# Kernel tuning notes

Measured on AMD Instinct MI355X. Metric: run time of the kernel, lower is better.

Reference implementation:

```python
import jax, jax.numpy as jnp
import numpy as np

N_HEAD, D_MODEL, DQ, DK, DV = 16, 1024, 64, 64, 64
B, LQ, LK = 2, 2048, 2048
EPS = 1e-3


def setup_inputs() -> dict:
    key = jax.random.key(0)
    ks = jax.random.split(key, 8)
    v = jax.random.normal(ks[0], (B, LK, D_MODEL), jnp.float32)
    k = jax.random.normal(ks[1], (B, LK, D_MODEL), jnp.float32)
    q = jax.random.normal(ks[2], (B, LQ, D_MODEL), jnp.float32)
    mask = jax.random.randint(ks[3], (B, LQ, LK), 0, 2).astype(bool)
    # xavier_normal for [n_head, d_model, d*]: fan_in=d_model, fan_out=d* (per torch, last two dims)
    def xav(kk, shape):
        std = np.sqrt(2.0 / (shape[-2] + shape[-1]))
        return jax.random.normal(kk, shape, jnp.float32) * std
    w_q = xav(ks[4], (N_HEAD, D_MODEL, DQ))
    w_k = xav(ks[5], (N_HEAD, D_MODEL, DK))
    w_v = xav(ks[6], (N_HEAD, D_MODEL, DV))
    # output linear: torch default init; use uniform(-1/sqrt(fan_in), ..)
    fan_in = N_HEAD * DV
    bound = 1.0 / np.sqrt(fan_in)
    kw, kb = jax.random.split(ks[7])
    w_o = jax.random.uniform(kw, (fan_in, D_MODEL), jnp.float32, -bound, bound)
    b_o = jax.random.uniform(kb, (D_MODEL,), jnp.float32, -bound, bound)
    gamma = jnp.ones((D_MODEL,), jnp.float32)
    beta = jnp.zeros((D_MODEL,), jnp.float32)
    return {"v": v, "k": k, "q": q, "mask": mask, "w_q": w_q, "w_k": w_k,
            "w_v": w_v, "w_o": w_o, "b_o": b_o, "gamma": gamma, "beta": beta}


def _layer_norm(x, gamma, beta):
    mean = jnp.mean(x, axis=-1, keepdims=True)
    # torch.std default is unbiased (ddof=1); eps added to std (not var)
    std = jnp.std(x, axis=-1, keepdims=True, ddof=1)
    return (x - mean) / (std + EPS) * gamma + beta


def reference(v, k, q, mask, w_q, w_k, w_v, w_o, b_o, gamma, beta):
    residual = k  # source uses k as residual
    # per-head projections: [h, b, l, d*]
    qh = jnp.einsum('bld,hde->hble', q, w_q)
    kh = jnp.einsum('bld,hde->hble', k, w_k)
    vh = jnp.einsum('bld,hde->hble', v, w_v)
    scale = 1.0 / np.sqrt(DK)
    scores = jnp.einsum('hbqe,hbke->hbqk', qh, kh) * scale  # [h,b,Lq,Lk]
    scores = jnp.where(mask[None], -jnp.inf, scores)
    attn = jax.nn.softmax(scores, axis=-1)
    out = jnp.einsum('hbqk,hbke->hbqe', attn, vh)  # [h,b,Lq,dv]
    # cat(split(out, batch, dim=0), dim=-1): heads concatenated on last dim
    out = out.transpose(1, 2, 0, 3).reshape(out.shape[1], out.shape[2], -1)
    out = out @ w_o + b_o
    x = out + residual  # dropout is identity in eval
    return _layer_norm(x, gamma, beta)
```

## Files before the change

### kernel.cpp

```cpp
#include <hip/hip_runtime.h>
#include <math.h>

typedef __bf16 bf16_t;
typedef bf16_t bf16x8 __attribute__((ext_vector_type(8)));
typedef float  f32x4  __attribute__((ext_vector_type(4)));
typedef unsigned short u16;
typedef u16 ushortx4 __attribute__((ext_vector_type(4)));
typedef unsigned long long u64;

#define MFMA16(a, b, c) __builtin_amdgcn_mfma_f32_16x16x32_bf16((a), (b), (c), 0, 0, 0)

__device__ __forceinline__ u16 f2bf(float f) {
    unsigned int u = __float_as_uint(f);
    u = (u + 0x7fffu + ((u >> 16) & 1u)) >> 16;
    return (u16)u;
}

__device__ __forceinline__ void gld16(const u16* g, u16* l) {
    __builtin_amdgcn_global_load_lds(
        (const __attribute__((address_space(1))) void*)g,
        (__attribute__((address_space(3))) void*)l, 16, 0, 0);
}


__global__ __launch_bounds__(256) void k_cvt3(const float* __restrict__ q,
                                              const float* __restrict__ k,
                                              const float* __restrict__ v,
                                              u16* __restrict__ qb,
                                              u16* __restrict__ kb,
                                              u16* __restrict__ vb) {
    int i = blockIdx.x * 256 + threadIdx.x;
    int sel = blockIdx.y;
    const float* src = sel == 0 ? q : (sel == 1 ? k : v);
    u16* dst = sel == 0 ? qb : (sel == 1 ? kb : vb);
    float4 val = ((const float4*)src)[i];
    ushortx4 r;
    r[0] = f2bf(val.x); r[1] = f2bf(val.y); r[2] = f2bf(val.z); r[3] = f2bf(val.w);
    ((ushortx4*)dst)[i] = r;
}

__global__ __launch_bounds__(256) void k_tcvt3(const float* __restrict__ w_q,
                                               const float* __restrict__ w_k,
                                               const float* __restrict__ w_v,
                                               u16* __restrict__ wqt,
                                               u16* __restrict__ wkt,
                                               u16* __restrict__ wvt) {
    __shared__ float tile[32][33];
    int z = blockIdx.z, h = z & 15, sel = z >> 4;
    const float* src = (sel == 0 ? w_q : (sel == 1 ? w_k : w_v));
    u16* dst = (sel == 0 ? wqt : (sel == 1 ? wkt : wvt));
    int r0 = blockIdx.x * 32, c0 = blockIdx.y * 32;
    int tx = threadIdx.x & 31, ty = threadIdx.x >> 5;
    const float* s = src + ((size_t)h * 1024 + r0) * 64 + c0;
#pragma unroll
    for (int i = 0; i < 4; ++i) tile[ty + i * 8][tx] = s[(ty + i * 8) * 64 + tx];
    __syncthreads();
    u16* d = dst + ((size_t)h * 64 + c0) * 1024 + r0;
#pragma unroll
    for (int i = 0; i < 4; ++i) d[(ty + i * 8) * 1024 + tx] = f2bf(tile[tx][ty + i * 8]);
}

__global__ __launch_bounds__(256) void k_tcvt(const float* __restrict__ src,
                                              u16* __restrict__ dst, int R, int C) {
    __shared__ float tile[32][33];
    int r0 = blockIdx.x * 32, c0 = blockIdx.y * 32;
    int tx = threadIdx.x & 31, ty = threadIdx.x >> 5;
    const float* s = src + (size_t)r0 * C + c0;
#pragma unroll
    for (int i = 0; i < 4; ++i) tile[ty + i * 8][tx] = s[(ty + i * 8) * (size_t)C + tx];
    __syncthreads();
    u16* d = dst + (size_t)c0 * R + r0;
#pragma unroll
    for (int i = 0; i < 4; ++i) d[(ty + i * 8) * (size_t)R + tx] = f2bf(tile[tx][ty + i * 8]);
}

__global__ __launch_bounds__(256) void k_packmask(const int* __restrict__ mask,
                                                  u64* __restrict__ mask64) {
    int bid = blockIdx.x;
    int ktg = bid & 7, q4 = (bid >> 3) & 511, b = bid >> 12;
    int wave = threadIdx.x >> 6, lane = threadIdx.x & 63;
    int q = q4 * 4 + wave;
    const int* mp = mask + ((size_t)(b * 2048 + q)) * 2048 + ktg * 256 + lane;
#pragma unroll
    for (int i = 0; i < 4; ++i) {
        int m = mp[i * 64];
        u64 bal = __ballot(m != 0);
        if (lane == 0) mask64[((size_t)(b * 32 + ktg * 4 + i)) * 2048 + q] = bal;
    }
}

#define GEMM_CORE(Ablk, Bblk, ACC)                                                    \
    int c0 = wave * 2;                                                                \
    const u16* Ag0 = Ablk + (size_t)(c0 * 16 + l15) * 1024 + quad * 8;                \
    const u16* Ag1 = Ablk + (size_t)((c0 + 1) * 16 + l15) * 1024 + quad * 8;          \
    const u16* Bg0 = Bblk + (size_t)(c0 * 16 + l15) * 1024 + quad * 8;                \
    const u16* Bg1 = Bblk + (size_t)((c0 + 1) * 16 + l15) * 1024 + quad * 8;          \
    gld16(Ag0, As + c0 * 512); gld16(Ag1, As + (c0 + 1) * 512);                       \
    gld16(Bg0, Bs + c0 * 512); gld16(Bg1, Bs + (c0 + 1) * 512);                       \
    __syncthreads();                                                                  \
    int buf = 0;                                                                      \
    for (int ks = 0; ks < 32; ++ks) {                                                 \
        if (ks < 31) {                                                                \
            int k0 = (ks + 1) * 32;                                                   \
            gld16(Ag0 + k0, As + (buf ^ 1) * 4096 + c0 * 512);                        \
            gld16(Ag1 + k0, As + (buf ^ 1) * 4096 + (c0 + 1) * 512);                  \
            gld16(Bg0 + k0, Bs + (buf ^ 1) * 4096 + c0 * 512);                        \
            gld16(Bg1 + k0, Bs + (buf ^ 1) * 4096 + (c0 + 1) * 512);                  \
        }                                                                             \
        bf16x8 af[4], bfr[4];                                                         \
        _Pragma("unroll")                                                             \
        for (int i = 0; i < 4; ++i)                                                   \
            af[i] = *(const bf16x8*)(As + buf * 4096 + (wy * 4 + i) * 512 + lane * 8);\
        _Pragma("unroll")                                                             \
        for (int j = 0; j < 4; ++j)                                                   \
            bfr[j] = *(const bf16x8*)(Bs + buf * 4096 + (wx * 4 + j) * 512 + lane * 8);\
        _Pragma("unroll")                                                             \
        for (int i = 0; i < 4; ++i)                                                   \
            _Pragma("unroll")                                                         \
            for (int j = 0; j < 4; ++j) ACC[i][j] = MFMA16(af[i], bfr[j], ACC[i][j]); \
        __syncthreads();                                                              \
        buf ^= 1;                                                                     \
    }

__global__ __launch_bounds__(256) void k_proj(
    const u16* __restrict__ qb, const u16* __restrict__ kb, const u16* __restrict__ vb,
    const u16* __restrict__ wqt, const u16* __restrict__ wkt, const u16* __restrict__ wvt,
    u16* __restrict__ oq, u16* __restrict__ okh, u16* __restrict__ ovt) {
    __shared__ __align__(16) u16 smem[18432];
    u16* As = smem;
    u16* Bs = smem + 8192;
    int z = blockIdx.y, gx = blockIdx.x;
    int bm, bn;
    const u16 *A, *B;
    if (z == 0)      { bm = gx >> 3; bn = gx & 7; A = qb; B = wqt; }
    else if (z == 1) { bm = gx >> 3; bn = gx & 7; A = kb; B = wkt; }
    else             { bm = gx & 7; bn = gx >> 3; A = wvt; B = vb; }
    A += (size_t)bm * 128 * 1024;
    B += (size_t)bn * 128 * 1024;
    int tid = threadIdx.x, wave = tid >> 6, lane = tid & 63;
    int wy = wave >> 1, wx = wave & 1, l15 = lane & 15, quad = lane >> 4;
    f32x4 acc[4][4] = {};
    GEMM_CORE(A, B, acc)
    u16* ep = smem + wave * 4608;
    float mulf = (z == 0) ? 0.18033688011112042f : 1.0f;
#pragma unroll
    for (int i = 0; i < 4; ++i)
#pragma unroll
        for (int j = 0; j < 4; ++j)
#pragma unroll
            for (int r = 0; r < 4; ++r)
                ep[(i * 16 + quad * 4 + r) * 72 + j * 16 + l15] = f2bf(acc[i][j][r] * mulf);
    int rl = lane >> 3, cg = lane & 7;
    if (z < 2) {
        int hh = bn * 2 + wx;
        int m0 = bm * 128 + wy * 64;
        int bb = m0 >> 11, l0 = m0 & 2047;
        u16* O = (z ? okh : oq) + ((size_t)((hh * 2 + bb) * 2048 + l0)) * 64;
#pragma unroll
        for (int s = 0; s < 8; ++s) {
            int row = s * 8 + rl;
            uint4 v = *(const uint4*)(ep + row * 72 + cg * 8);
            *(uint4*)(O + (size_t)row * 64 + cg * 8) = v;
        }
    } else {
        int m0 = bm * 128 + wy * 64;
        int hh = m0 >> 6;
        int n0 = bn * 128 + wx * 64;
        int bb = n0 >> 11, l0 = n0 & 2047;
        u16* O = ovt + (size_t)(hh * 2 + bb) * 131072 + (size_t)(m0 & 63) * 2048 + l0;
#pragma unroll
        for (int s = 0; s < 8; ++s) {
            int row = s * 8 + rl;
            uint4 v = *(const uint4*)(ep + row * 72 + cg * 8);
            *(uint4*)(O + (size_t)row * 2048 + cg * 8) = v;
        }
    }
}

__global__ __launch_bounds__(256) void k_out(
    const u16* __restrict__ ao, const u16* __restrict__ wot,
    const float* __restrict__ bo, const float* __restrict__ resid,
    float* __restrict__ xb) {
    __shared__ __align__(16) u16 smem[18432];
    u16* As = smem;
    u16* Bs = smem + 8192;
    int gx = blockIdx.x, bm = gx >> 3, bn = gx & 7;
    const u16* A = ao + (size_t)bm * 128 * 1024;
    const u16* B = wot + (size_t)bn * 128 * 1024;
    int tid = threadIdx.x, wave = tid >> 6, lane = tid & 63;
    int wy = wave >> 1, wx = wave & 1, l15 = lane & 15, quad = lane >> 4;
    f32x4 acc[4][4] = {};
    GEMM_CORE(A, B, acc)
    float* epf = (float*)(smem) + wave * 2176;
    int cgf = lane & 15, rlf = lane >> 4;
    int mbase = bm * 128 + wy * 64, nbase = bn * 128 + wx * 64;
#pragma unroll
    for (int cc = 0; cc < 2; ++cc) {
#pragma unroll
        for (int i2 = 0; i2 < 2; ++i2)
#pragma unroll
            for (int j = 0; j < 4; ++j)
#pragma unroll
                for (int r = 0; r < 4; ++r)
                    epf[(i2 * 16 + quad * 4 + r) * 68 + j * 16 + l15] =
                        acc[cc * 2 + i2][j][r];
#pragma unroll
        for (int s = 0; s < 8; ++s) {
            int row = s * 4 + rlf;
            f32x4 v = *(const f32x4*)(epf + row * 68 + cgf * 4);
            int m = mbase + cc * 32 + row, n = nbase + cgf * 4;
            float4 rsd = *(const float4*)(resid + (size_t)m * 1024 + n);
            float4 bo4 = *(const float4*)(bo + n);
            float4 o;
            o.x = v[0] + bo4.x + rsd.x;
            o.y = v[1] + bo4.y + rsd.y;
            o.z = v[2] + bo4.z + rsd.z;
            o.w = v[3] + bo4.w + rsd.w;
            *(float4*)(xb + (size_t)m * 1024 + n) = o;
        }
    }
}

__global__ __launch_bounds__(512) void k_attn(
    const u16* __restrict__ qh, const u16* __restrict__ kh,
    const u16* __restrict__ vt, const u64* __restrict__ mask64,
    u16* __restrict__ ao) {
    int qt = blockIdx.x, hb = blockIdx.y;
    int h = hb >> 1, b = hb & 1;
    int tid = threadIdx.x, wave = tid >> 6, lane = tid & 63;
    int l15 = lane & 15, quad = lane >> 4;

    __shared__ __align__(16) u16 Ks[2][4096], Vs[2][4096];
    __shared__ __align__(16) u16 Pb[8][16][72];

    int qrow0 = qt * 128 + wave * 16;
    const u16* Qp = qh + ((size_t)(hb * 2048) + qrow0 + l15) * 64 + quad * 8;
    bf16x8 qf0 = *(const bf16x8*)Qp;
    bf16x8 qf1 = *(const bf16x8*)(Qp + 32);

    int tK = wave >> 1, hK = wave & 1;
    const u16* Kg = kh + (size_t)hb * 131072 + (size_t)(tK * 16 + l15) * 64 + hK * 32 + quad * 8;
    const u16* Vg = vt + (size_t)hb * 131072 + (size_t)(tK * 16 + l15) * 2048 + hK * 32 + quad * 8;
    const u64* Mp = mask64 + (size_t)b * 65536 + qrow0 + l15;

    float l_lane = 0.f;
    f32x4 o[4] = {};

    gld16(Kg, &Ks[0][wave * 512]);
    gld16(Vg, &Vs[0][wave * 512]);
    u64 mw_cur = Mp[0];
    __syncthreads();
    int buf = 0;
    for (int kt = 0; kt < 32; ++kt) {
        u64 mw_nxt = 0;
        if (kt < 31) {
            gld16(Kg + (size_t)(kt + 1) * 4096, &Ks[buf ^ 1][wave * 512]);
            gld16(Vg + (size_t)(kt + 1) * 64, &Vs[buf ^ 1][wave * 512]);
            mw_nxt = Mp[(size_t)(kt + 1) * 2048];
        }
        f32x4 st[4] = {};
#pragma unroll
        for (int t = 0; t < 4; ++t) {
            bf16x8 k0 = *(const bf16x8*)&Ks[buf][(t * 2 + 0) * 512 + lane * 8];
            bf16x8 k1 = *(const bf16x8*)&Ks[buf][(t * 2 + 1) * 512 + lane * 8];
            st[t] = MFMA16(k0, qf0, st[t]);
            st[t] = MFMA16(k1, qf1, st[t]);
        }
        unsigned int w0 = (unsigned int)(mw_cur >> (quad * 4));
        unsigned int w1 = (unsigned int)(mw_cur >> (32 + quad * 4));
#pragma unroll
        for (int r = 0; r < 4; ++r) {
            st[0][r] = ((w0 >> r) & 1u) ? -3e30f : st[0][r];
            st[1][r] = ((w0 >> (16 + r)) & 1u) ? -3e30f : st[1][r];
            st[2][r] = ((w1 >> r) & 1u) ? -3e30f : st[2][r];
            st[3][r] = ((w1 >> (16 + r)) & 1u) ? -3e30f : st[3][r];
        }
#pragma unroll
        for (int t = 0; t < 4; ++t) {
            float p0 = __builtin_amdgcn_exp2f(st[t][0]);
            float p1 = __builtin_amdgcn_exp2f(st[t][1]);
            float p2 = __builtin_amdgcn_exp2f(st[t][2]);
            float p3 = __builtin_amdgcn_exp2f(st[t][3]);
            l_lane += (p0 + p1) + (p2 + p3);
            uint2 pk;
            pk.x = (__float_as_uint(p1) & 0xffff0000u) | (__float_as_uint(p0) >> 16);
            pk.y = (__float_as_uint(p3) & 0xffff0000u) | (__float_as_uint(p2) >> 16);
            *(uint2*)&Pb[wave][l15][t * 16 + quad * 4] = pk;
        }
#pragma unroll
        for (int kc = 0; kc < 2; ++kc) {
            bf16x8 pf = *(const bf16x8*)&Pb[wave][l15][kc * 32 + quad * 8];
#pragma unroll
            for (int t = 0; t < 4; ++t) {
                bf16x8 vf = *(const bf16x8*)&Vs[buf][(t * 2 + kc) * 512 + lane * 8];
                o[t] = MFMA16(pf, vf, o[t]);
            }
        }
        mw_cur = mw_nxt;
        __syncthreads();
        buf ^= 1;
    }
    float ls = l_lane;
    ls += __shfl_xor(ls, 16, 64);
    ls += __shfl_xor(ls, 32, 64);
    float inv = 1.0f / ls;
    f32x4 ivr;
#pragma unroll
    for (int r = 0; r < 4; ++r) ivr[r] = __shfl(inv, quad * 4 + r, 16);
#pragma unroll
    for (int t = 0; t < 4; ++t)
#pragma unroll
        for (int r = 0; r < 4; ++r)
            Pb[wave][quad * 4 + r][t * 16 + l15] = f2bf(o[t][r] * ivr[r]);
    int rl = lane >> 3, cg = lane & 7;
#pragma unroll
    for (int s = 0; s < 2; ++s) {
        int row = s * 8 + rl;
        uint4 v = *(const uint4*)&Pb[wave][row][cg * 8];
        *(uint4*)(ao + ((size_t)(b * 2048 + qrow0 + row)) * 1024 + h * 64 + cg * 8) = v;
    }
}

__global__ __launch_bounds__(256) void k_ln(const float* __restrict__ x,
                                            const float* __restrict__ gamma,
                                            const float* __restrict__ beta,
                                            float* __restrict__ out) {
    int row = blockIdx.x;
    const float* xr = x + (size_t)row * 1024;
    float4 v = ((const float4*)xr)[threadIdx.x];
    float s = v.x + v.y + v.z + v.w;
    float ss = v.x * v.x + v.y * v.y + v.z * v.z + v.w * v.w;
#pragma unroll
    for (int off = 32; off; off >>= 1) {
        s += __shfl_down(s, off, 64);
        ss += __shfl_down(ss, off, 64);
    }
    __shared__ float sb[8];
    int wave = threadIdx.x >> 6, lane = threadIdx.x & 63;
    if (lane == 0) { sb[wave] = s; sb[4 + wave] = ss; }
    __syncthreads();
    s = sb[0] + sb[1] + sb[2] + sb[3];
    ss = sb[4] + sb[5] + sb[6] + sb[7];
    float mean = s * (1.0f / 1024.0f);
    float var = fmaxf((ss - 1024.0f * mean * mean) * (1.0f / 1023.0f), 0.f);
    float inv = 1.0f / (sqrtf(var) + 1e-3f);
    float4 g = ((const float4*)gamma)[threadIdx.x];
    float4 bt = ((const float4*)beta)[threadIdx.x];
    float4 o;
    o.x = (v.x - mean) * inv * g.x + bt.x;
    o.y = (v.y - mean) * inv * g.y + bt.y;
    o.z = (v.z - mean) * inv * g.z + bt.z;
    o.w = (v.w - mean) * inv * g.w + bt.w;
    ((float4*)(out + (size_t)row * 1024))[threadIdx.x] = o;
}

extern "C" void kernel_launch(void* const* d_in, const int* in_sizes, int n_in,
                              void* d_out, int out_size, void* d_ws, size_t ws_size,
                              hipStream_t stream) {
    const float* v_in  = (const float*)d_in[0];
    const float* k_in  = (const float*)d_in[1];
    const float* q_in  = (const float*)d_in[2];
    const int*   mask  = (const int*)d_in[3];
    const float* w_q   = (const float*)d_in[4];
    const float* w_k   = (const float*)d_in[5];
    const float* w_v   = (const float*)d_in[6];
    const float* w_o   = (const float*)d_in[7];
    const float* b_o   = (const float*)d_in[8];
    const float* gamma = (const float*)d_in[9];
    const float* beta  = (const float*)d_in[10];
    float* out = (float*)d_out;

    char* ws = (char*)d_ws;
    const size_t MB = 1ull << 20;
    u16* qb  = (u16*)(ws + 0 * MB);
    u16* kb  = (u16*)(ws + 8 * MB);
    u16* vb  = (u16*)(ws + 16 * MB);
    u16* wqt = (u16*)(ws + 24 * MB);
    u16* wkt = (u16*)(ws + 26 * MB);
    u16* wvt = (u16*)(ws + 28 * MB);
    u16* wot = (u16*)(ws + 30 * MB);
    u16* qh  = (u16*)(ws + 32 * MB);
    u16* kh  = (u16*)(ws + 40 * MB);
    u16* vt  = (u16*)(ws + 48 * MB);
    u16* ao  = (u16*)(ws + 56 * MB);
    u64* mask64 = (u64*)(ws + 64 * MB);
    float* xb = (float*)(ws + 64 * MB);

    k_cvt3<<<dim3(4096, 3), dim3(256), 0, stream>>>(q_in, k_in, v_in, qb, kb, vb);
    k_tcvt3<<<dim3(32, 2, 48), dim3(256), 0, stream>>>(w_q, w_k, w_v, wqt, wkt, wvt);
    k_tcvt<<<dim3(32, 32), dim3(256), 0, stream>>>(w_o, wot, 1024, 1024);
    k_packmask<<<dim3(8192), dim3(256), 0, stream>>>(mask, mask64);
    k_proj<<<dim3(256, 3), dim3(256), 0, stream>>>(qb, kb, vb, wqt, wkt, wvt, qh, kh, vt);
    k_attn<<<dim3(16, 32), dim3(512), 0, stream>>>(qh, kh, vt, mask64, ao);
    k_out<<<dim3(256), dim3(256), 0, stream>>>(ao, wot, b_o, k_in, xb);
    k_ln<<<dim3(4096), dim3(256), 0, stream>>>(xb, gamma, beta, out);
}
```

Measured before the change: 303.2 us.

## Process two query row-tiles per wave in attention to reuse K/V fragments

The attention kernel now runs 4 waves per block instead of 8, and each wave handles 32 query rows as two 16-row halves. K and V fragments are loaded from LDS into registers once per key tile and reused for both halves, which roughly halves LDS read traffic per query row. Each wave issues twice as many global-to-LDS loads. The cost is higher register pressure and fewer waves per block to hide latency, which could lower occupancy.

```diff
diff --git a/kernel.cpp b/kernel.cpp
--- a/kernel.cpp
+++ b/kernel.cpp
@@ -221,7 +221,7 @@
     }
 }
 
-__global__ __launch_bounds__(512) void k_attn(
+__global__ __launch_bounds__(256) void k_attn(
     const u16* __restrict__ qh, const u16* __restrict__ kh,
     const u16* __restrict__ vt, const u64* __restrict__ mask64,
     u16* __restrict__ ao) {
@@ -231,94 +231,119 @@
     int l15 = lane & 15, quad = lane >> 4;
 
     __shared__ __align__(16) u16 Ks[2][4096], Vs[2][4096];
-    __shared__ __align__(16) u16 Pb[8][16][72];
-
-    int qrow0 = qt * 128 + wave * 16;
+    __shared__ __align__(16) u16 Pb[4][2][16][72];
+
+    int qrow0 = qt * 128 + wave * 32;
     const u16* Qp = qh + ((size_t)(hb * 2048) + qrow0 + l15) * 64 + quad * 8;
-    bf16x8 qf0 = *(const bf16x8*)Qp;
-    bf16x8 qf1 = *(const bf16x8*)(Qp + 32);
-
-    int tK = wave >> 1, hK = wave & 1;
-    const u16* Kg = kh + (size_t)hb * 131072 + (size_t)(tK * 16 + l15) * 64 + hK * 32 + quad * 8;
-    const u16* Vg = vt + (size_t)hb * 131072 + (size_t)(tK * 16 + l15) * 2048 + hK * 32 + quad * 8;
+    bf16x8 qf[2][2];
+    qf[0][0] = *(const bf16x8*)Qp;
+    qf[0][1] = *(const bf16x8*)(Qp + 32);
+    qf[1][0] = *(const bf16x8*)(Qp + 1024);
+    qf[1][1] = *(const bf16x8*)(Qp + 1024 + 32);
+
+    int c0 = wave * 2;
+    int rA = (c0 >> 1) * 16 + l15, dA = (c0 & 1) * 32 + quad * 8;
+    int rB = ((c0 + 1) >> 1) * 16 + l15, dB = ((c0 + 1) & 1) * 32 + quad * 8;
+    const u16* Kg0 = kh + (size_t)hb * 131072 + (size_t)rA * 64 + dA;
+    const u16* Kg1 = kh + (size_t)hb * 131072 + (size_t)rB * 64 + dB;
+    const u16* Vg0 = vt + (size_t)hb * 131072 + (size_t)rA * 2048 + dA;
+    const u16* Vg1 = vt + (size_t)hb * 131072 + (size_t)rB * 2048 + dB;
     const u64* Mp = mask64 + (size_t)b * 65536 + qrow0 + l15;
 
-    float l_lane = 0.f;
-    f32x4 o[4] = {};
-
-    gld16(Kg, &Ks[0][wave * 512]);
-    gld16(Vg, &Vs[0][wave * 512]);
-    u64 mw_cur = Mp[0];
+    float l_lane[2] = {0.f, 0.f};
+    f32x4 o[2][4] = {};
+
+    gld16(Kg0, &Ks[0][c0 * 512]);
+    gld16(Kg1, &Ks[0][(c0 + 1) * 512]);
+    gld16(Vg0, &Vs[0][c0 * 512]);
+    gld16(Vg1, &Vs[0][(c0 + 1) * 512]);
+    u64 mw0 = Mp[0], mw1 = Mp[16];
     __syncthreads();
     int buf = 0;
     for (int kt = 0; kt < 32; ++kt) {
-        u64 mw_nxt = 0;
+        u64 mwn0 = 0, mwn1 = 0;
         if (kt < 31) {
-            gld16(Kg + (size_t)(kt + 1) * 4096, &Ks[buf ^ 1][wave * 512]);
-            gld16(Vg + (size_t)(kt + 1) * 64, &Vs[buf ^ 1][wave * 512]);
-            mw_nxt = Mp[(size_t)(kt + 1) * 2048];
-        }
-        f32x4 st[4] = {};
-#pragma unroll
-        for (int t = 0; t < 4; ++t) {
-            bf16x8 k0 = *(const bf16x8*)&Ks[buf][(t * 2 + 0) * 512 + lane * 8];
-            bf16x8 k1 = *(const bf16x8*)&Ks[buf][(t * 2 + 1) * 512 + lane * 8];
-            st[t] = MFMA16(k0, qf0, st[t]);
-            st[t] = MFMA16(k1, qf1, st[t]);
-        }
-        unsigned int w0 = (unsigned int)(mw_cur >> (quad * 4));
-        unsigned int w1 = (unsigned int)(mw_cur >> (32 + quad * 4));
-#pragma unroll
-        for (int r = 0; r < 4; ++r) {
-            st[0][r] = ((w0 >> r) & 1u) ? -3e30f : st[0][r];
-            st[1][r] = ((w0 >> (16 + r)) & 1u) ? -3e30f : st[1][r];
-            st[2][r] = ((w1 >> r) & 1u) ? -3e30f : st[2][r];
-            st[3][r] = ((w1 >> (16 + r)) & 1u) ? -3e30f : st[3][r];
-        }
-#pragma unroll
-        for (int t = 0; t < 4; ++t) {
-            float p0 = __builtin_amdgcn_exp2f(st[t][0]);
-            float p1 = __builtin_amdgcn_exp2f(st[t][1]);
-            float p2 = __builtin_amdgcn_exp2f(st[t][2]);
-            float p3 = __builtin_amdgcn_exp2f(st[t][3]);
-            l_lane += (p0 + p1) + (p2 + p3);
-            uint2 pk;
-            pk.x = (__float_as_uint(p1) & 0xffff0000u) | (__float_as_uint(p0) >> 16);
-            pk.y = (__float_as_uint(p3) & 0xffff0000u) | (__float_as_uint(p2) >> 16);
-            *(uint2*)&Pb[wave][l15][t * 16 + quad * 4] = pk;
-        }
-#pragma unroll
-        for (int kc = 0; kc < 2; ++kc) {
-            bf16x8 pf = *(const bf16x8*)&Pb[wave][l15][kc * 32 + quad * 8];
+            gld16(Kg0 + (size_t)(kt + 1) * 4096, &Ks[buf ^ 1][c0 * 512]);
+            gld16(Kg1 + (size_t)(kt + 1) * 4096, &Ks[buf ^ 1][(c0 + 1) * 512]);
+            gld16(Vg0 + (size_t)(kt + 1) * 64, &Vs[buf ^ 1][c0 * 512]);
+            gld16(Vg1 + (size_t)(kt + 1) * 64, &Vs[buf ^ 1][(c0 + 1) * 512]);
+            mwn0 = Mp[(size_t)(kt + 1) * 2048];
+            mwn1 = Mp[(size_t)(kt + 1) * 2048 + 16];
+        }
+        bf16x8 kf[8], vf[8];
+#pragma unroll
+        for (int c = 0; c < 8; ++c) kf[c] = *(const bf16x8*)&Ks[buf][c * 512 + lane * 8];
+#pragma unroll
+        for (int c = 0; c < 8; ++c) vf[c] = *(const bf16x8*)&Vs[buf][c * 512 + lane * 8];
+#pragma unroll
+        for (int hf = 0; hf < 2; ++hf) {
+            u64 mw = hf ? mw1 : mw0;
+            f32x4 st[4] = {};
 #pragma unroll
             for (int t = 0; t < 4; ++t) {
-                bf16x8 vf = *(const bf16x8*)&Vs[buf][(t * 2 + kc) * 512 + lane * 8];
-                o[t] = MFMA16(pf, vf, o[t]);
+                st[t] = MFMA16(kf[t * 2], qf[hf][0], st[t]);
+                st[t] = MFMA16(kf[t * 2 + 1], qf[hf][1], st[t]);
             }
-        }
-        mw_cur = mw_nxt;
+            unsigned int w0 = (unsigned int)(mw >> (quad * 4));
+            unsigned int w1 = (unsigned int)(mw >> (32 + quad * 4));
+#pragma unroll
+            for (int r = 0; r < 4; ++r) {
+                st[0][r] = ((w0 >> r) & 1u) ? -3e30f : st[0][r];
+                st[1][r] = ((w0 >> (16 + r)) & 1u) ? -3e30f : st[1][r];
+                st[2][r] = ((w1 >> r) & 1u) ? -3e30f : st[2][r];
+                st[3][r] = ((w1 >> (16 + r)) & 1u) ? -3e30f : st[3][r];
+            }
+            float ll = 0.f;
+#pragma unroll
+            for (int t = 0; t < 4; ++t) {
+                float p0 = __builtin_amdgcn_exp2f(st[t][0]);
+                float p1 = __builtin_amdgcn_exp2f(st[t][1]);
+                float p2 = __builtin_amdgcn_exp2f(st[t][2]);
+                float p3 = __builtin_amdgcn_exp2f(st[t][3]);
+                ll += (p0 + p1) + (p2 + p3);
+                uint2 pk;
+                pk.x = (__float_as_uint(p1) & 0xffff0000u) | (__float_as_uint(p0) >> 16);
+                pk.y = (__float_as_uint(p3) & 0xffff0000u) | (__float_as_uint(p2) >> 16);
+                *(uint2*)&Pb[wave][hf][l15][t * 16 + quad * 4] = pk;
+            }
+            l_lane[hf] += ll;
+#pragma unroll
+            for (int kc = 0; kc < 2; ++kc) {
+                bf16x8 pf = *(const bf16x8*)&Pb[wave][hf][l15][kc * 32 + quad * 8];
+#pragma unroll
+                for (int t = 0; t < 4; ++t)
+                    o[hf][t] = MFMA16(pf, vf[t * 2 + kc], o[hf][t]);
+            }
+        }
+        mw0 = mwn0; mw1 = mwn1;
         __syncthreads();
         buf ^= 1;
     }
-    float ls = l_lane;
-    ls += __shfl_xor(ls, 16, 64);
-    ls += __shfl_xor(ls, 32, 64);
-    float inv = 1.0f / ls;
-    f32x4 ivr;
-#pragma unroll
-    for (int r = 0; r < 4; ++r) ivr[r] = __shfl(inv, quad * 4 + r, 16);
-#pragma unroll
-    for (int t = 0; t < 4; ++t)
-#pragma unroll
-        for (int r = 0; r < 4; ++r)
-            Pb[wave][quad * 4 + r][t * 16 + l15] = f2bf(o[t][r] * ivr[r]);
+#pragma unroll
+    for (int hf = 0; hf < 2; ++hf) {
+        float ls = l_lane[hf];
+        ls += __shfl_xor(ls, 16, 64);
+        ls += __shfl_xor(ls, 32, 64);
+        float inv = 1.0f / ls;
+        f32x4 ivr;
+#pragma unroll
+        for (int r = 0; r < 4; ++r) ivr[r] = __shfl(inv, quad * 4 + r, 16);
+#pragma unroll
+        for (int t = 0; t < 4; ++t)
+#pragma unroll
+            for (int r = 0; r < 4; ++r)
+                Pb[wave][hf][quad * 4 + r][t * 16 + l15] = f2bf(o[hf][t][r] * ivr[r]);
+    }
     int rl = lane >> 3, cg = lane & 7;
 #pragma unroll
-    for (int s = 0; s < 2; ++s) {
-        int row = s * 8 + rl;
-        uint4 v = *(const uint4*)&Pb[wave][row][cg * 8];
-        *(uint4*)(ao + ((size_t)(b * 2048 + qrow0 + row)) * 1024 + h * 64 + cg * 8) = v;
-    }
+    for (int hf = 0; hf < 2; ++hf)
+#pragma unroll
+        for (int s = 0; s < 2; ++s) {
+            int row = s * 8 + rl;
+            uint4 v = *(const uint4*)&Pb[wave][hf][row][cg * 8];
+            *(uint4*)(ao + ((size_t)(b * 2048 + qrow0 + hf * 16 + row)) * 1024 +
+                      h * 64 + cg * 8) = v;
+        }
 }
 
 __global__ __launch_bounds__(256) void k_ln(const float* __restrict__ x,
@@ -391,7 +416,7 @@
     k_tcvt<<<dim3(32, 32), dim3(256), 0, stream>>>(w_o, wot, 1024, 1024);
     k_packmask<<<dim3(8192), dim3(256), 0, stream>>>(mask, mask64);
     k_proj<<<dim3(256, 3), dim3(256), 0, stream>>>(qb, kb, vb, wqt, wkt, wvt, qh, kh, vt);
-    k_attn<<<dim3(16, 32), dim3(512), 0, stream>>>(qh, kh, vt, mask64, ao);
+    k_attn<<<dim3(16, 32), dim3(256), 0, stream>>>(qh, kh, vt, mask64, ao);
     k_out<<<dim3(256), dim3(256), 0, stream>>>(ao, wot, b_o, k_in, xb);
     k_ln<<<dim3(4096), dim3(256), 0, stream>>>(xb, gamma, beta, out);
 }
```

After: 308.1 us. No clear change (+1.6%).
